# Optimization experiments

Measured on AMD Instinct MI355X. Metric: run time of the kernel, lower is better.

Reference implementation:

```python
import jax, jax.numpy as jnp
import numpy as np

BN_EPS = 1e-5

def setup_inputs() -> dict:
    key = jax.random.key(0)
    ks = jax.random.split(key, 7)
    B, D, A = 16384, 768, 51
    s = 1.0 / np.sqrt(D)
    return {
        "x": jax.random.normal(ks[0], (B, D), dtype=jnp.float32),
        "W_embed": jax.random.uniform(ks[1], (D, D), minval=-s, maxval=s, dtype=jnp.float32),
        "b_embed": jax.random.uniform(ks[2], (D,), minval=-s, maxval=s, dtype=jnp.float32),
        "W_attr": jax.random.uniform(ks[3], (A, D), minval=-s, maxval=s, dtype=jnp.float32),  # stacked per-attribute (dim->1) heads
        "b_attr": jax.random.uniform(ks[4], (A,), minval=-s, maxval=s, dtype=jnp.float32),
        "gamma": jnp.ones((A,), dtype=jnp.float32),
        "beta": jnp.zeros((A,), dtype=jnp.float32),
    }

def reference(x, W_embed, b_embed, W_attr, b_attr, gamma, beta):
    # word_embed: Linear(dim, dim)
    h = x @ W_embed.T + b_embed                      # [B, D]
    # fused per-attribute heads: cat of attr_num (dim->1) linears == one (dim->attr_num) matmul
    logits = h @ W_attr.T + b_attr                    # [B, A]
    # BatchNorm1d (training mode: batch statistics, biased variance)
    mean = jnp.mean(logits, axis=0)
    var = jnp.var(logits, axis=0)
    y = (logits - mean) * jax.lax.rsqrt(var + BN_EPS) * gamma + beta
    return y
```

## Files before the change

### kernel.cpp

```cpp
#include <hip/hip_runtime.h>

typedef _Float16 halfx8 __attribute__((ext_vector_type(8)));
typedef float floatx4 __attribute__((ext_vector_type(4)));
typedef float floatx2 __attribute__((ext_vector_type(2)));

#define GLOBAL_AS __attribute__((address_space(1)))
#define LDS_AS __attribute__((address_space(3)))

__device__ __forceinline__ void async_copy_16(const void* g, void* l) {
    __builtin_amdgcn_global_load_lds((GLOBAL_AS void*)g, (LDS_AS void*)l, 16, 0, 0);
}

#define PM 16384
#define PD 768
#define PA 51
#define NBLK 256u


__device__ __forceinline__ size_t fragidx(int a, int d) {
    return (size_t)(d >> 5) * 2048 + (size_t)(a >> 4) * 512
         + (size_t)((a & 15) | (((d >> 3) & 3) << 4)) * 8 + (d & 7);
}

__global__ __launch_bounds__(256) void prep_kernel(
    const float* __restrict__ We, const float* __restrict__ be,
    const float* __restrict__ Wa, const float* __restrict__ ba,
    _Float16* __restrict__ wfrag, float* __restrict__ bc,
    unsigned int* __restrict__ counter)
{
    const int wave = threadIdx.x >> 6;
    const int lane = threadIdx.x & 63;
    const int Wu = __builtin_amdgcn_readfirstlane((int)blockIdx.x * 4 + wave);

    if (Wu < 312) {
        const int pair = Wu / 12;
        const int dchunk = Wu - pair * 12;
        const int a0 = pair * 2;
        const bool has1 = (a0 + 1 < PA);
        const int d = dchunk * 64 + lane;
        const float* wa0 = Wa + (size_t)a0 * PD;
        const float* wa1 = Wa + (size_t)(has1 ? a0 + 1 : a0) * PD;
        float acc0 = 0.f, acc1 = 0.f;
        #pragma unroll 32
        for (int k = 0; k < PD; ++k) {
            float w = We[(size_t)k * PD + d];
            acc0 = fmaf(w, wa0[k], acc0);
            acc1 = fmaf(w, wa1[k], acc1);
        }
        wfrag[fragidx(a0, d)] = (_Float16)acc0;
        if (has1) wfrag[fragidx(a0 + 1, d)] = (_Float16)acc1;
    } else if (Wu < 325) {
        const int r = PA + (Wu - 312);
        #pragma unroll
        for (int j = 0; j < 12; ++j)
            wfrag[fragidx(r, j * 64 + lane)] = (_Float16)0.f;
    } else if (Wu < 376) {
        const int a = Wu - 325;
        float p = 0.f;
        #pragma unroll
        for (int j = 0; j < 12; ++j) {
            int k = j * 64 + lane;
            p = fmaf(Wa[(size_t)a * PD + k], be[k], p);
        }
        #pragma unroll
        for (int off = 32; off; off >>= 1) p += __shfl_down(p, off);
        if (lane == 0) bc[a] = p + ba[a];
    } else if (Wu == 376) {
        if (lane == 0) *counter = 0u;
    }
}

__global__ void __launch_bounds__(256, 1) gemm_bn_kernel(
    const float* __restrict__ X,
    const _Float16* __restrict__ Wfrag,
    const float* __restrict__ bc,
    const float* __restrict__ gamma,
    const float* __restrict__ beta,
    float* __restrict__ out,
    unsigned long long* __restrict__ part,
    unsigned int* __restrict__ counter)
{
    __shared__ __attribute__((aligned(16))) _Float16 Bh[24 * 4 * 512];
    __shared__ __attribute__((aligned(16))) float Atile[4][3][16 * 64];
    __shared__ float s_sum[64];
    __shared__ float s_ssq[64];
    __shared__ float redS[256];
    __shared__ float redQ[256];
    __shared__ float s_scale[64];
    __shared__ float s_shift[64];

    const int tid = threadIdx.x;
    const int wave = tid >> 6;
    const int lane = tid & 63;
    const int quad = lane >> 4;
    const int l16 = lane & 15;
    const int m0 = (int)blockIdx.x * 64 + wave * 16;

    if (tid < 64) { s_sum[tid] = 0.f; s_ssq[tid] = 0.f; }

    #pragma unroll
    for (int j = 0; j < 24; ++j) {
        int ch = wave * 24 + j;
        async_copy_16((const char*)Wfrag + (size_t)ch * 1024 + (size_t)lane * 16,
                      (char*)Bh + (size_t)ch * 1024);
    }
    asm volatile("" ::: "memory");

    auto stageA = [&](int buf, int kt) {
        #pragma unroll
        for (int j = 0; j < 4; ++j) {
            int r = j * 4 + (lane >> 4);
            int c = lane & 15;
            int csw = (c & 8) | ((c & 7) ^ (r & 7));
            async_copy_16(X + (size_t)(m0 + r) * PD + kt + csw * 4,
                          (char*)&Atile[wave][buf][0] + (size_t)(j * 64) * 16);
        }
        asm volatile("" ::: "memory");
    };

    floatx4 acc[4];
    #pragma unroll
    for (int n = 0; n < 4; ++n) acc[n] = (floatx4){0.f, 0.f, 0.f, 0.f};

    stageA(0, 0);
    stageA(1, 64);
    stageA(2, 128);
    asm volatile("s_waitcnt vmcnt(12)\n\ts_barrier" ::: "memory");

    #pragma unroll
    for (int mm = 0; mm < 12; ++mm) {
        if (mm <= 9)       asm volatile("s_waitcnt vmcnt(8)" ::: "memory");
        else if (mm == 10) asm volatile("s_waitcnt vmcnt(4)" ::: "memory");
        else               asm volatile("s_waitcnt vmcnt(0)" ::: "memory");
        const float* At = &Atile[wave][mm % 3][0];
        #pragma unroll
        for (int km = 0; km < 2; ++km) {
            const int ks = mm * 2 + km;
            int cc = km * 8 + quad * 2;
            int s3 = l16 & 7;
            floatx4 p0 = *(const floatx4*)&At[l16 * 64 + (((cc & 8) | ((cc & 7) ^ s3)) << 2)];
            floatx4 p1 = *(const floatx4*)&At[l16 * 64 + ((((cc + 1) & 8) | (((cc + 1) & 7) ^ s3)) << 2)];
            halfx8 af;
            af[0] = (_Float16)p0[0]; af[1] = (_Float16)p0[1];
            af[2] = (_Float16)p0[2]; af[3] = (_Float16)p0[3];
            af[4] = (_Float16)p1[0]; af[5] = (_Float16)p1[1];
            af[6] = (_Float16)p1[2]; af[7] = (_Float16)p1[3];
            #pragma unroll
            for (int n = 0; n < 4; ++n) {
                halfx8 bf = *(const halfx8*)&Bh[(size_t)(ks * 4 + n) * 512 + (size_t)lane * 8];
                acc[n] = __builtin_amdgcn_mfma_f32_16x16x32_f16(af, bf, acc[n], 0, 0, 0);
            }
        }
        if (mm + 3 < 12) stageA(mm % 3, (mm + 3) * 64);
    }

    float keep[4][4];
    #pragma unroll
    for (int n = 0; n < 4; ++n) {
        int col = n * 16 + l16;
        if (col < PA) {
            float bv = bc[col];
            float ps = 0.f, pss = 0.f;
            #pragma unroll
            for (int r = 0; r < 4; ++r) {
                float v = acc[n][r] + bv;
                keep[n][r] = v;
                ps += v; pss += v * v;
            }
            atomicAdd(&s_sum[col], ps);
            atomicAdd(&s_ssq[col], pss);
        }
    }
    __syncthreads();

    if (tid < 64) {
        union { floatx2 f; unsigned long long u; } v;
        v.f = (floatx2){s_sum[tid], s_ssq[tid]};
        __hip_atomic_store(&part[(size_t)blockIdx.x * 64 + tid], v.u,
                           __ATOMIC_RELAXED, __HIP_MEMORY_SCOPE_AGENT);
    }
    __syncthreads();

    if (tid == 0) {
        __hip_atomic_fetch_add(counter, 1u, __ATOMIC_ACQ_REL, __HIP_MEMORY_SCOPE_AGENT);
        while (__hip_atomic_load(counter, __ATOMIC_RELAXED, __HIP_MEMORY_SCOPE_AGENT) < NBLK)
            __builtin_amdgcn_s_sleep(8);
        (void)__hip_atomic_load(counter, __ATOMIC_ACQUIRE, __HIP_MEMORY_SCOPE_AGENT);
    }
    __syncthreads();

    {
        const int col = tid & 63;
        const int q = tid >> 6;
        float rs = 0.f, rq = 0.f;
        #pragma unroll 8
        for (int i = q * 64; i < q * 64 + 64; ++i) {
            union { unsigned long long u; floatx2 f; } v;
            v.u = __hip_atomic_load(&part[(size_t)i * 64 + col],
                                    __ATOMIC_RELAXED, __HIP_MEMORY_SCOPE_AGENT);
            rs += v.f[0]; rq += v.f[1];
        }
        redS[tid] = rs; redQ[tid] = rq;
    }
    __syncthreads();

    const float invB = 1.0f / (float)PM;
    if (tid < PA) {
        float s  = redS[tid] + redS[64 + tid] + redS[128 + tid] + redS[192 + tid];
        float ss = redQ[tid] + redQ[64 + tid] + redQ[128 + tid] + redQ[192 + tid];
        float mean = s * invB;
        float var  = ss * invB - mean * mean;
        float inv  = rsqrtf(var + 1e-5f);
        float sc = gamma[tid] * inv;
        s_scale[tid] = sc;
        s_shift[tid] = beta[tid] - mean * sc;
    }
    __syncthreads();

    #pragma unroll
    for (int n = 0; n < 4; ++n) {
        int col = n * 16 + l16;
        if (col < PA) {
            float sc = s_scale[col], sh = s_shift[col];
            int rowb = m0 + quad * 4;
            #pragma unroll
            for (int r = 0; r < 4; ++r)
                out[(size_t)(rowb + r) * PA + col] = keep[n][r] * sc + sh;
        }
    }
}

extern "C" void kernel_launch(void* const* d_in, const int* in_sizes, int n_in,
                              void* d_out, int out_size, void* d_ws, size_t ws_size,
                              hipStream_t stream) {
    const float* x       = (const float*)d_in[0];
    const float* W_embed = (const float*)d_in[1];
    const float* b_embed = (const float*)d_in[2];
    const float* W_attr  = (const float*)d_in[3];
    const float* b_attr  = (const float*)d_in[4];
    const float* gamma   = (const float*)d_in[5];
    const float* beta    = (const float*)d_in[6];
    float* out = (float*)d_out;

    char* ws = (char*)d_ws;
    _Float16* wfrag       = (_Float16*)(ws);
    float* bc             = (float*)(ws + 98304);
    unsigned int* counter = (unsigned int*)(ws + 98560);
    unsigned long long* part = (unsigned long long*)(ws + 98816);

    prep_kernel<<<95, 256, 0, stream>>>(W_embed, b_embed, W_attr, b_attr,
                                        wfrag, bc, counter);
    gemm_bn_kernel<<<256, 256, 0, stream>>>(x, wfrag, bc, gamma, beta, out,
                                            part, counter);
}
```

Baseline: 147.5 us.

## Replace grid-wide spin barrier with last-block reduction and separate BN kernel

The fused GEMM+BN kernel, which spun on a global counter until all blocks arrived, is split in two. The GEMM kernel now writes raw logits to workspace. The last block to finish reduces the per-block partial sums and writes scale/shift, and a new elementwise kernel applies the normalization. This removes the grid-wide busy wait and its reliance on all 256 blocks being co-resident, at the cost of an extra kernel launch and a write-then-read round trip of the logits through global memory.

```diff
diff --git a/kernel.cpp b/kernel.cpp
--- a/kernel.cpp
+++ b/kernel.cpp
@@ -70,15 +70,16 @@
     }
 }
 
-__global__ void __launch_bounds__(256, 1) gemm_bn_kernel(
+__global__ void __launch_bounds__(256, 1) gemm_kernel(
     const float* __restrict__ X,
     const _Float16* __restrict__ Wfrag,
     const float* __restrict__ bc,
     const float* __restrict__ gamma,
     const float* __restrict__ beta,
-    float* __restrict__ out,
+    float* __restrict__ logits,
     unsigned long long* __restrict__ part,
-    unsigned int* __restrict__ counter)
+    unsigned int* __restrict__ counter,
+    float* __restrict__ ss)
 {
     __shared__ __attribute__((aligned(16))) _Float16 Bh[24 * 4 * 512];
     __shared__ __attribute__((aligned(16))) float Atile[4][3][16 * 64];
@@ -86,8 +87,7 @@
     __shared__ float s_ssq[64];
     __shared__ float redS[256];
     __shared__ float redQ[256];
-    __shared__ float s_scale[64];
-    __shared__ float s_shift[64];
+    __shared__ int s_last;
 
     const int tid = threadIdx.x;
     const int wave = tid >> 6;
@@ -154,17 +154,17 @@
         if (mm + 3 < 12) stageA(mm % 3, (mm + 3) * 64);
     }
 
-    float keep[4][4];
     #pragma unroll
     for (int n = 0; n < 4; ++n) {
         int col = n * 16 + l16;
         if (col < PA) {
             float bv = bc[col];
             float ps = 0.f, pss = 0.f;
+            int rowb = m0 + quad * 4;
             #pragma unroll
             for (int r = 0; r < 4; ++r) {
                 float v = acc[n][r] + bv;
-                keep[n][r] = v;
+                logits[(size_t)(rowb + r) * PA + col] = v;
                 ps += v; pss += v * v;
             }
             atomicAdd(&s_sum[col], ps);
@@ -182,14 +182,12 @@
     __syncthreads();
 
     if (tid == 0) {
-        __hip_atomic_fetch_add(counter, 1u, __ATOMIC_ACQ_REL, __HIP_MEMORY_SCOPE_AGENT);
-        while (__hip_atomic_load(counter, __ATOMIC_RELAXED, __HIP_MEMORY_SCOPE_AGENT) < NBLK)
-            __builtin_amdgcn_s_sleep(8);
-        (void)__hip_atomic_load(counter, __ATOMIC_ACQUIRE, __HIP_MEMORY_SCOPE_AGENT);
-    }
-    __syncthreads();
-
-    {
+        unsigned int old = __hip_atomic_fetch_add(counter, 1u, __ATOMIC_ACQ_REL,
+                                                  __HIP_MEMORY_SCOPE_AGENT);
+        s_last = (old == NBLK - 1u);
+    }
+    __syncthreads();
+    if (s_last) {
         const int col = tid & 63;
         const int q = tid >> 6;
         float rs = 0.f, rq = 0.f;
@@ -201,33 +199,44 @@
             rs += v.f[0]; rq += v.f[1];
         }
         redS[tid] = rs; redQ[tid] = rq;
-    }
-    __syncthreads();
-
-    const float invB = 1.0f / (float)PM;
-    if (tid < PA) {
-        float s  = redS[tid] + redS[64 + tid] + redS[128 + tid] + redS[192 + tid];
-        float ss = redQ[tid] + redQ[64 + tid] + redQ[128 + tid] + redQ[192 + tid];
-        float mean = s * invB;
-        float var  = ss * invB - mean * mean;
-        float inv  = rsqrtf(var + 1e-5f);
-        float sc = gamma[tid] * inv;
-        s_scale[tid] = sc;
-        s_shift[tid] = beta[tid] - mean * sc;
-    }
-    __syncthreads();
-
-    #pragma unroll
-    for (int n = 0; n < 4; ++n) {
-        int col = n * 16 + l16;
-        if (col < PA) {
-            float sc = s_scale[col], sh = s_shift[col];
-            int rowb = m0 + quad * 4;
-            #pragma unroll
-            for (int r = 0; r < 4; ++r)
-                out[(size_t)(rowb + r) * PA + col] = keep[n][r] * sc + sh;
-        }
-    }
+        __syncthreads();
+        const float invB = 1.0f / (float)PM;
+        if (tid < PA) {
+            float s  = redS[tid] + redS[64 + tid] + redS[128 + tid] + redS[192 + tid];
+            float sq = redQ[tid] + redQ[64 + tid] + redQ[128 + tid] + redQ[192 + tid];
+            float mean = s * invB;
+            float var  = sq * invB - mean * mean;
+            float inv  = rsqrtf(var + 1e-5f);
+            float sc = gamma[tid] * inv;
+            ss[tid] = sc;
+            ss[64 + tid] = beta[tid] - mean * sc;
+        }
+    }
+}
+
+__global__ __launch_bounds__(256) void bn_kernel(
+    const float* __restrict__ logits,
+    const float* __restrict__ ss,
+    float* __restrict__ out)
+{
+    __shared__ float sc[64];
+    __shared__ float sh[64];
+    const int t = threadIdx.x;
+    if (t < 64) { sc[t] = ss[t]; sh[t] = ss[64 + t]; }
+    __syncthreads();
+
+    const int idx = (int)blockIdx.x * 256 + t;
+    floatx4 v = ((const floatx4*)logits)[idx];
+    int c0 = (idx * 4) % 51;
+    int c1 = c0 + 1; if (c1 >= 51) c1 -= 51;
+    int c2 = c1 + 1; if (c2 >= 51) c2 -= 51;
+    int c3 = c2 + 1; if (c3 >= 51) c3 -= 51;
+    floatx4 r;
+    r[0] = v[0] * sc[c0] + sh[c0];
+    r[1] = v[1] * sc[c1] + sh[c1];
+    r[2] = v[2] * sc[c2] + sh[c2];
+    r[3] = v[3] * sc[c3] + sh[c3];
+    ((floatx4*)out)[idx] = r;
 }
 
 extern "C" void kernel_launch(void* const* d_in, const int* in_sizes, int n_in,
@@ -247,9 +256,12 @@
     float* bc             = (float*)(ws + 98304);
     unsigned int* counter = (unsigned int*)(ws + 98560);
     unsigned long long* part = (unsigned long long*)(ws + 98816);
+    float* ssbuf          = (float*)(ws + 229888);
+    float* logits         = (float*)(ws + 230400);
 
     prep_kernel<<<95, 256, 0, stream>>>(W_embed, b_embed, W_attr, b_attr,
                                         wfrag, bc, counter);
-    gemm_bn_kernel<<<256, 256, 0, stream>>>(x, wfrag, bc, gamma, beta, out,
-                                            part, counter);
-}
+    gemm_kernel<<<256, 256, 0, stream>>>(x, wfrag, bc, gamma, beta,
+                                         logits, part, counter, ssbuf);
+    bn_kernel<<<816, 256, 0, stream>>>(logits, ssbuf, out);
+}
```

New measurement: 141.6 us. -4.0%, faster.
